# Kernel optimization log

Hardware: AMD Instinct MI355X
Metric: run time of the kernel (lower is better)

The kernel has to match this reference:

```python
import jax, jax.numpy as jnp
import numpy as np
import math

EPS = 1e-8
MIN_RADIUS = 0.1
SINH_MAX = math.asinh(2.0 ** 15)
CURV = 1.0                     # exp(clamp(log(1.0), log(0.1), log(10)))
IMAGE_ALPHA = 0.25             # exp(clamp(log(1/4), max=0))
TEXT_ALPHA = 1.0 / 0.6         # exp(log(1/0.6)), frozen
LOGIT_SCALE = 1.0 / 0.07       # exp(clamp(log(1/0.07), max=4.6052))
ENTAIL_WEIGHT = 0.2


def exp_map0(x, curv):
    # MERU exponential map at the Lorentz-model origin (space components only).
    rc = jnp.sqrt(curv) * jnp.linalg.norm(x, axis=-1, keepdims=True)
    sinh_in = jnp.clip(rc, EPS, SINH_MAX)
    return jnp.sinh(sinh_in) * x / jnp.maximum(rc, EPS)


def pairwise_dist(x, y, curv):
    # x: (B,H,W,D) image feats on hyperboloid; y: (C,D) text protos. -> (B,H,W,C)
    x_time = jnp.sqrt(1.0 / curv + jnp.sum(x * x, axis=-1))   # (B,H,W)
    y_time = jnp.sqrt(1.0 / curv + jnp.sum(y * y, axis=-1))   # (C,)
    inner = jnp.einsum('bhwd,cd->bhwc', x, y) - x_time[..., None] * y_time
    c_xyl = -curv * inner
    return jnp.arccosh(jnp.maximum(c_xyl, 1.0 + EPS)) / jnp.sqrt(curv)


def oxy_angle(x, y, curv):
    # Exterior angle at x between origin->x and x->y geodesics. x,y: (...,D) -> (...,)
    x_time = jnp.sqrt(1.0 / curv + jnp.sum(x * x, axis=-1))
    y_time = jnp.sqrt(1.0 / curv + jnp.sum(y * y, axis=-1))
    c_xyl = curv * (jnp.sum(x * y, axis=-1) - x_time * y_time)
    acos_num = y_time + c_xyl * x_time
    acos_den = jnp.linalg.norm(x, axis=-1) * jnp.sqrt(jnp.maximum(c_xyl * c_xyl - 1.0, 0.0))
    acos_in = acos_num / (acos_den + EPS)
    return jnp.arccos(jnp.clip(acos_in, -1.0 + EPS, 1.0 - EPS))


def half_aperture(x, curv):
    asin_in = 2.0 * MIN_RADIUS / (jnp.linalg.norm(x, axis=-1) * jnp.sqrt(curv) + EPS)
    return jnp.arcsin(jnp.clip(asin_in, -1.0 + EPS, 1.0 - EPS))


def _forward(feats, text_protos, labels, mask):
    curv = jnp.float32(CURV)
    img = exp_map0(feats * IMAGE_ALPHA, curv)          # (B,H,W,D)
    txt = exp_map0(text_protos * TEXT_ALPHA, curv)     # (C,D)

    dist = pairwise_dist(img, txt, curv)               # (B,H,W,C)
    proto = txt[labels]                                # (B,H,W,D) gather by GT class
    angle = oxy_angle(proto, img, curv)                # (B,H,W)
    aperture = half_aperture(proto, curv)              # (B,H,W)

    logits = LOGIT_SCALE * (-dist)                     # scale * image_logits
    logp = jax.nn.log_softmax(logits, axis=-1)
    nll = -jnp.take_along_axis(logp, labels[..., None], axis=-1)[..., 0]

    valid = (~mask).astype(jnp.float32)                # mask==1 means ignore
    n_valid = jnp.maximum(jnp.sum(valid), 1.0)
    sup_loss = jnp.sum(nll * valid) / n_valid

    ent = jnp.maximum(angle - aperture, 0.0)
    entail_loss = jnp.sum(ent * valid) / n_valid

    return sup_loss + ENTAIL_WEIGHT * entail_loss


def setup_inputs() -> dict:
    key = jax.random.key(0)
    k1, k2, k3, k4 = jax.random.split(key, 4)
    B, H, W, D, C = 2, 512, 512, 64, 151
    feats = jax.random.normal(k1, (B, H, W, D), dtype=jnp.float32)
    text_protos = jax.random.normal(k2, (C, D), dtype=jnp.float32)
    labels = jax.random.randint(k3, (B, H, W), 0, C, dtype=jnp.int32)
    mask = jax.random.randint(k4, (B, H, W), 0, 2, dtype=jnp.int32).astype(bool)
    return {"feats": feats, "text_protos": text_protos, "labels": labels, "mask": mask}


def reference(feats, text_protos, labels, mask):
    return _forward(feats, text_protos, labels, mask)
```

## Files before the change

kernel.cpp:

```cpp
#include <hip/hip_runtime.h>
#include <math.h>

#define EPSF 1e-8f
#define SINH_MAXF 11.090354888959125f
#define IMAGE_ALPHA 0.25f
#define TEXT_ALPHA (1.0f/0.6f)
#define LOGIT_SCALE (1.0f/0.07f)
#define LN2F 0.6931471805599453f
#define SLN (LOGIT_SCALE*LN2F)
#define ENTAIL_WEIGHT 0.2f
#define NCLS 151
#define NPAD 160
#define DIM 64
#define NBLK 2048

#define LMIN_OFF 8
#define YT_OFF 16
#define XN_OFF (YT_OFF + NPAD)
#define AP_OFF (XN_OFF + NPAD)
#define BT_OFF 512
#define BLK_OFF (BT_OFF + NPAD*DIM/2)

#if __has_builtin(__builtin_amdgcn_exp2f)
#define EXP2F(x) __builtin_amdgcn_exp2f(x)
#else
#define EXP2F(x) __expf((x) * LN2F)
#endif

typedef __attribute__((ext_vector_type(8))) short bf16x8;
typedef __attribute__((ext_vector_type(4))) float f32x4;

__device__ inline unsigned short f2bf(float f) {
    unsigned int u = __float_as_uint(f);
    return (unsigned short)((u + 0x7FFFu + ((u >> 16) & 1u)) >> 16);
}
__device__ inline unsigned int pack_bf_trunc(float hi, float lo) {
    return __builtin_amdgcn_perm(__float_as_uint(hi), __float_as_uint(lo), 0x07060302u);
}
__device__ inline float sel4(const float* a, int i) {
    return i == 0 ? a[0] : i == 1 ? a[1] : i == 2 ? a[2] : a[3];
}
__device__ inline int isel4(const int* a, int i) {
    return i == 0 ? a[0] : i == 1 ? a[1] : i == 2 ? a[2] : a[3];
}

__global__ __launch_bounds__(256) void proto_kernel(const float* __restrict__ protos,
                                                    float* __restrict__ ws) {
    int tid = threadIdx.x;
    int grp = tid >> 4, li = tid & 15;
    unsigned int* btu = (unsigned int*)(ws + BT_OFF);
    __shared__ float sYT[NPAD];
    #pragma unroll 2
    for (int t = 0; t < 10; t++) {
        int c = t * 16 + grp;
        float4 p4 = make_float4(0.f, 0.f, 0.f, 0.f);
        if (c < NCLS) p4 = ((const float4*)protos)[c * 16 + li];
        float vx = p4.x * TEXT_ALPHA, vy = p4.y * TEXT_ALPHA,
              vz = p4.z * TEXT_ALPHA, vw = p4.w * TEXT_ALPHA;
        float n2 = vx*vx + vy*vy + vz*vz + vw*vw;
        #pragma unroll
        for (int m = 8; m >= 1; m >>= 1) n2 += __shfl_xor(n2, m, 64);
        float rc = __builtin_amdgcn_sqrtf(n2);
        float rr = fminf(fmaxf(rc, EPSF), SINH_MAXF);
        float e = __expf(rr);
        float sh = 0.5f * (e - __builtin_amdgcn_rcpf(e));
        float sc = sh * __builtin_amdgcn_rcpf(fmaxf(rc, EPSF));
        unsigned int u0, u1;
        float yt, xn, ap;
        if (c < NCLS) {
            u0 = (unsigned int)f2bf(sc * vx) | ((unsigned int)f2bf(sc * vy) << 16);
            u1 = (unsigned int)f2bf(sc * vz) | ((unsigned int)f2bf(sc * vw) << 16);
            xn = sc * rc;
            yt = __builtin_amdgcn_sqrtf(fmaf(xn, xn, 1.f));
            float ai = fminf(fmaxf(0.2f / (xn + EPSF), -1.f + EPSF), 1.f - EPSF);
            ap = asinf(ai);
        } else {
            u0 = 0u; u1 = 0u; yt = 2e18f; xn = 1.f; ap = 0.f;
        }
        int unit = t * 128 + (li >> 3) * 64 + ((li >> 1) & 3) * 16 + grp;
        btu[unit * 4 + (li & 1) * 2]     = u0;
        btu[unit * 4 + (li & 1) * 2 + 1] = u1;
        if (li == 0) {
            ws[YT_OFF + c] = yt; ws[XN_OFF + c] = xn; ws[AP_OFF + c] = ap;
            sYT[c] = yt;
        }
    }
    __syncthreads();
    if (tid < 64) {
        float m = 1e30f;
        for (int c = tid; c < NCLS; c += 64) m = fminf(m, sYT[c]);
        #pragma unroll
        for (int k = 32; k >= 1; k >>= 1) m = fminf(m, __shfl_xor(m, k, 64));
        if (tid == 0) ws[LMIN_OFF] = __log2f(2.f * m);
    }
}

struct PixA { bf16x8 q0, q1; float xt, Q; };

__device__ inline PixA stage_pixel(const float4* fp, float lmin2) {
    float4 f0 = fp[0], f1 = fp[1], f2 = fp[8], f3 = fp[9];
    float n2r = f0.x*f0.x + f0.y*f0.y + f0.z*f0.z + f0.w*f0.w
              + f1.x*f1.x + f1.y*f1.y + f1.z*f1.z + f1.w*f1.w
              + f2.x*f2.x + f2.y*f2.y + f2.z*f2.z + f2.w*f2.w
              + f3.x*f3.x + f3.y*f3.y + f3.z*f3.z + f3.w*f3.w;
    n2r += __shfl_xor(n2r, 16, 64);
    n2r += __shfl_xor(n2r, 32, 64);
    float rc = IMAGE_ALPHA * __builtin_amdgcn_sqrtf(n2r);
    float rr = fminf(fmaxf(rc, EPSF), SINH_MAXF);
    float e = __expf(rr);
    float sh = 0.5f * (e - __builtin_amdgcn_rcpf(e));
    float sc = sh * __builtin_amdgcn_rcpf(fmaxf(rc, EPSF));
    float xn = sc * rc;
    float k = sc * IMAGE_ALPHA;
    PixA r;
    r.xt = __builtin_amdgcn_sqrtf(fmaf(xn, xn, 1.f));
    r.Q = LOGIT_SCALE * (lmin2 - __log2f(r.xt + xn) - 1.0f);
    unsigned int* q0u = (unsigned int*)&r.q0;
    unsigned int* q1u = (unsigned int*)&r.q1;
    q0u[0] = pack_bf_trunc(k*f0.y, k*f0.x);
    q0u[1] = pack_bf_trunc(k*f0.w, k*f0.z);
    q0u[2] = pack_bf_trunc(k*f1.y, k*f1.x);
    q0u[3] = pack_bf_trunc(k*f1.w, k*f1.z);
    q1u[0] = pack_bf_trunc(k*f2.y, k*f2.x);
    q1u[1] = pack_bf_trunc(k*f2.w, k*f2.z);
    q1u[2] = pack_bf_trunc(k*f3.y, k*f3.x);
    q1u[3] = pack_bf_trunc(k*f3.w, k*f3.z);
    return r;
}

__global__ __launch_bounds__(256) void main_kernel(
    const float* __restrict__ feats, const int* __restrict__ labels,
    const unsigned char* __restrict__ mask, const float* __restrict__ wsro,
    float4* __restrict__ blkout, int nchunk)
{
    __shared__ uint4 sBT[1280];
    __shared__ float sYT[NPAD];
    int tid = threadIdx.x;
    const uint4* btg = (const uint4*)(wsro + BT_OFF);
    #pragma unroll
    for (int k = 0; k < 5; k++) sBT[tid + k * 256] = btg[tid + k * 256];
    if (tid < NPAD) sYT[tid] = wsro[YT_OFF + tid];
    __syncthreads();

    int wid = tid >> 6, lane = tid & 63;
    int cn = lane & 15, g = lane >> 4;
    float lmin2 = wsro[LMIN_OFF];

    float v_nll = 0.f, v_ent = 0.f, valid = 0.f;

    for (int chunk = blockIdx.x; chunk < nchunk; chunk += NBLK) {
        int wavebase = (chunk * 4 + wid) * 32;
        int pix0 = wavebase + cn, pix1 = pix0 + 16;

        PixA A0 = stage_pixel((const float4*)(feats + (size_t)pix0 * DIM + g * 8), lmin2);
        PixA A1 = stage_pixel((const float4*)(feats + (size_t)pix1 * DIM + g * 8), lmin2);
        int lab0 = labels[pix0], lab1 = labels[pix1];

        float xtr0[4], Q0[4], xtr1[4], Q1[4];
        int lr0[4], lr1[4];
        #pragma unroll
        for (int r = 0; r < 4; r++) {
            int src = g * 4 + r;
            xtr0[r] = __shfl(A0.xt, src, 64); Q0[r] = __shfl(A0.Q, src, 64);
            lr0[r]  = __shfl(lab0, src, 64);
            xtr1[r] = __shfl(A1.xt, src, 64); Q1[r] = __shfl(A1.Q, src, 64);
            lr1[r]  = __shfl(lab1, src, 64);
        }

        float ss0[4] = {0,0,0,0}, ss1[4] = {0,0,0,0};
        float sv0[4] = {0,0,0,0}, sv1[4] = {0,0,0,0};

        #pragma unroll 2
        for (int t = 0; t < 10; t++) {
            uint4 u0 = sBT[t * 128 + lane];
            uint4 u1 = sBT[t * 128 + 64 + lane];
            bf16x8 bq0 = __builtin_bit_cast(bf16x8, u0);
            bf16x8 bq1 = __builtin_bit_cast(bf16x8, u1);
            float yt = sYT[t * 16 + cn];
            int cls = t * 16 + cn;
            f32x4 d0 = {0,0,0,0}, d1 = {0,0,0,0};
            d0 = __builtin_amdgcn_mfma_f32_16x16x32_bf16(A0.q0, bq0, d0, 0, 0, 0);
            d0 = __builtin_amdgcn_mfma_f32_16x16x32_bf16(A0.q1, bq1, d0, 0, 0, 0);
            d1 = __builtin_amdgcn_mfma_f32_16x16x32_bf16(A1.q0, bq0, d1, 0, 0, 0);
            d1 = __builtin_amdgcn_mfma_f32_16x16x32_bf16(A1.q1, bq1, d1, 0, 0, 0);
            #pragma unroll
            for (int r = 0; r < 4; r++) {
                float c0 = fmaf(xtr0[r], yt, -d0[r]);
                if (lr0[r] == cls) sv0[r] = c0;
                ss0[r] += EXP2F(fmaf(-LOGIT_SCALE, __log2f(c0), Q0[r]));
                float c1 = fmaf(xtr1[r], yt, -d1[r]);
                if (lr1[r] == cls) sv1[r] = c1;
                ss1[r] += EXP2F(fmaf(-LOGIT_SCALE, __log2f(c1), Q1[r]));
            }
        }

        int gbase = lane & 48;
        float cx0[4], cx1[4];
        #pragma unroll
        for (int r = 0; r < 4; r++) {
            cx0[r] = __shfl(sv0[r], gbase + (lr0[r] & 15), 64);
            cx1[r] = __shfl(sv1[r], gbase + (lr1[r] & 15), 64);
        }
        #pragma unroll
        for (int k = 1; k < 16; k <<= 1) {
            #pragma unroll
            for (int r = 0; r < 4; r++) {
                ss0[r] += __shfl_xor(ss0[r], k, 64);
                ss1[r] += __shfl_xor(ss1[r], k, 64);
            }
        }

        if (cn < 4) {
            #pragma unroll
            for (int tile = 0; tile < 2; tile++) {
                float T   = tile ? sel4(ss1, cn) : sel4(ss0, cn);
                float cxl = tile ? sel4(cx1, cn) : sel4(cx0, cn);
                float xts = tile ? sel4(xtr1, cn) : sel4(xtr0, cn);
                float Q   = tile ? sel4(Q1, cn) : sel4(Q0, cn);
                int lb    = tile ? isel4(lr1, cn) : isel4(lr0, cn);
                int pr = wavebase + g * 4 + cn + tile * 16;
                float nll = LN2F * (__log2f(T) - Q + LOGIT_SCALE * __log2f(cxl));
                float pt = wsro[YT_OFF + lb], pn = wsro[XN_OFF + lb], ap = wsro[AP_OFF + lb];
                float num = fmaf(-cxl, pt, xts);
                float den = pn * __builtin_amdgcn_sqrtf(fmaxf(fmaf(cxl, cxl, -1.f), 0.f));
                float ain = num * __builtin_amdgcn_rcpf(den + EPSF);
                ain = fminf(fmaxf(ain, -1.f + EPSF), 1.f - EPSF);
                float ax = fabsf(ain);
                float p = fmaf(fmaf(fmaf(-0.0187293f, ax, 0.0742610f), ax, -0.2121144f),
                               ax, 1.5707288f);
                float rr = __builtin_amdgcn_sqrtf(1.f - ax) * p;
                float ac = ain < 0.f ? 3.14159265358979f - rr : rr;
                float ent = fmaxf(ac - ap, 0.f);
                float vl = mask[pr] ? 0.f : 1.f;
                v_nll += nll * vl; v_ent += ent * vl; valid += vl;
            }
        }
    }

    #pragma unroll
    for (int o = 32; o >= 1; o >>= 1) {
        v_nll += __shfl_down(v_nll, o, 64);
        v_ent += __shfl_down(v_ent, o, 64);
        valid += __shfl_down(valid, o, 64);
    }
    __shared__ float red[3][4];
    if (lane == 0) { red[0][wid] = v_nll; red[1][wid] = v_ent; red[2][wid] = valid; }
    __syncthreads();
    if (tid == 0) {
        float a = 0.f, b = 0.f, c = 0.f;
        #pragma unroll
        for (int w = 0; w < 4; w++) { a += red[0][w]; b += red[1][w]; c += red[2][w]; }
        blkout[blockIdx.x] = make_float4(a, b, c, 0.f);
    }
}

__global__ __launch_bounds__(1024) void reduce_kernel(const float4* __restrict__ blk,
                                                      float* __restrict__ out) {
    float a = 0.f, b = 0.f, c = 0.f;
    for (int i = threadIdx.x; i < NBLK; i += 1024) {
        float4 v = blk[i];
        a += v.x; b += v.y; c += v.z;
    }
    #pragma unroll
    for (int o = 32; o >= 1; o >>= 1) {
        a += __shfl_down(a, o, 64);
        b += __shfl_down(b, o, 64);
        c += __shfl_down(c, o, 64);
    }
    __shared__ float red[3][16];
    int wid = threadIdx.x >> 6, lane = threadIdx.x & 63;
    if (lane == 0) { red[0][wid] = a; red[1][wid] = b; red[2][wid] = c; }
    __syncthreads();
    if (threadIdx.x == 0) {
        float A = 0.f, B = 0.f, C = 0.f;
        #pragma unroll
        for (int w = 0; w < 16; w++) { A += red[0][w]; B += red[1][w]; C += red[2][w]; }
        float n = fmaxf(C, 1.f);
        out[0] = A / n + ENTAIL_WEIGHT * (B / n);
    }
}

extern "C" void kernel_launch(void* const* d_in, const int* in_sizes, int n_in,
                              void* d_out, int out_size, void* d_ws, size_t ws_size,
                              hipStream_t stream) {
    const float* feats  = (const float*)d_in[0];
    const float* protos = (const float*)d_in[1];
    const int* labels   = (const int*)d_in[2];
    const unsigned char* mask = (const unsigned char*)d_in[3];
    float* ws = (float*)d_ws;

    proto_kernel<<<1, 256, 0, stream>>>(protos, ws);

    int npix = in_sizes[2];
    int nchunk = npix / 128;
    main_kernel<<<NBLK, 256, 0, stream>>>(feats, labels, mask, ws,
                                          (float4*)(ws + BLK_OFF), nchunk);
    reduce_kernel<<<1, 1024, 0, stream>>>((const float4*)(ws + BLK_OFF), (float*)d_out);
}
```

Baseline: 212.3 us.

## Prefetch both chunks' inputs before LDS staging, two chunks per block

```diff
diff --git a/kernel.cpp b/kernel.cpp
--- a/kernel.cpp
+++ b/kernel.cpp
@@ -97,8 +97,8 @@
 
 struct PixA { bf16x8 q0, q1; float xt, Q; };
 
-__device__ inline PixA stage_pixel(const float4* fp, float lmin2) {
-    float4 f0 = fp[0], f1 = fp[1], f2 = fp[8], f3 = fp[9];
+__device__ __forceinline__ PixA stage_pixel_r(float4 f0, float4 f1, float4 f2, float4 f3,
+                                              float lmin2) {
     float n2r = f0.x*f0.x + f0.y*f0.y + f0.z*f0.z + f0.w*f0.w
               + f1.x*f1.x + f1.y*f1.y + f1.z*f1.z + f1.w*f1.w
               + f2.x*f2.x + f2.y*f2.y + f2.z*f2.z + f2.w*f2.w
@@ -128,7 +128,98 @@
     return r;
 }
 
-__global__ __launch_bounds__(256) void main_kernel(
+__device__ __forceinline__ void process_chunk(
+    float4 a00, float4 a01, float4 a02, float4 a03,
+    float4 a10, float4 a11, float4 a12, float4 a13,
+    int lab0, int lab1, unsigned char mk0, unsigned char mk1,
+    int lane, int cn, int g,
+    const uint4* sBT, const float* sYT, const float* __restrict__ wsro, float lmin2,
+    float& v_nll, float& v_ent, float& valid)
+{
+    PixA A0 = stage_pixel_r(a00, a01, a02, a03, lmin2);
+    PixA A1 = stage_pixel_r(a10, a11, a12, a13, lmin2);
+
+    float xtr0[4], Q0[4], xtr1[4], Q1[4];
+    int lr0[4], lr1[4];
+    #pragma unroll
+    for (int r = 0; r < 4; r++) {
+        int src = g * 4 + r;
+        xtr0[r] = __shfl(A0.xt, src, 64); Q0[r] = __shfl(A0.Q, src, 64);
+        lr0[r]  = __shfl(lab0, src, 64);
+        xtr1[r] = __shfl(A1.xt, src, 64); Q1[r] = __shfl(A1.Q, src, 64);
+        lr1[r]  = __shfl(lab1, src, 64);
+    }
+
+    float ss0[4] = {0,0,0,0}, ss1[4] = {0,0,0,0};
+    float sv0[4] = {0,0,0,0}, sv1[4] = {0,0,0,0};
+
+    #pragma unroll 2
+    for (int t = 0; t < 10; t++) {
+        uint4 u0 = sBT[t * 128 + lane];
+        uint4 u1 = sBT[t * 128 + 64 + lane];
+        bf16x8 bq0 = __builtin_bit_cast(bf16x8, u0);
+        bf16x8 bq1 = __builtin_bit_cast(bf16x8, u1);
+        float yt = sYT[t * 16 + cn];
+        int cls = t * 16 + cn;
+        f32x4 d0 = {0,0,0,0}, d1 = {0,0,0,0};
+        d0 = __builtin_amdgcn_mfma_f32_16x16x32_bf16(A0.q0, bq0, d0, 0, 0, 0);
+        d0 = __builtin_amdgcn_mfma_f32_16x16x32_bf16(A0.q1, bq1, d0, 0, 0, 0);
+        d1 = __builtin_amdgcn_mfma_f32_16x16x32_bf16(A1.q0, bq0, d1, 0, 0, 0);
+        d1 = __builtin_amdgcn_mfma_f32_16x16x32_bf16(A1.q1, bq1, d1, 0, 0, 0);
+        #pragma unroll
+        for (int r = 0; r < 4; r++) {
+            float c0 = fmaf(xtr0[r], yt, -d0[r]);
+            if (lr0[r] == cls) sv0[r] = c0;
+            ss0[r] += EXP2F(fmaf(-LOGIT_SCALE, __log2f(c0), Q0[r]));
+            float c1 = fmaf(xtr1[r], yt, -d1[r]);
+            if (lr1[r] == cls) sv1[r] = c1;
+            ss1[r] += EXP2F(fmaf(-LOGIT_SCALE, __log2f(c1), Q1[r]));
+        }
+    }
+
+    int gbase = lane & 48;
+    float cx0[4], cx1[4];
+    #pragma unroll
+    for (int r = 0; r < 4; r++) {
+        cx0[r] = __shfl(sv0[r], gbase + (lr0[r] & 15), 64);
+        cx1[r] = __shfl(sv1[r], gbase + (lr1[r] & 15), 64);
+    }
+    #pragma unroll
+    for (int k = 1; k < 16; k <<= 1) {
+        #pragma unroll
+        for (int r = 0; r < 4; r++) {
+            ss0[r] += __shfl_xor(ss0[r], k, 64);
+            ss1[r] += __shfl_xor(ss1[r], k, 64);
+        }
+    }
+
+    if (cn < 4) {
+        #pragma unroll
+        for (int tile = 0; tile < 2; tile++) {
+            float T   = tile ? sel4(ss1, cn) : sel4(ss0, cn);
+            float cxl = tile ? sel4(cx1, cn) : sel4(cx0, cn);
+            float xts = tile ? sel4(xtr1, cn) : sel4(xtr0, cn);
+            float Q   = tile ? sel4(Q1, cn) : sel4(Q0, cn);
+            int lb    = tile ? isel4(lr1, cn) : isel4(lr0, cn);
+            float nll = LN2F * (__log2f(T) - Q + LOGIT_SCALE * __log2f(cxl));
+            float pt = wsro[YT_OFF + lb], pn = wsro[XN_OFF + lb], ap = wsro[AP_OFF + lb];
+            float num = fmaf(-cxl, pt, xts);
+            float den = pn * __builtin_amdgcn_sqrtf(fmaxf(fmaf(cxl, cxl, -1.f), 0.f));
+            float ain = num * __builtin_amdgcn_rcpf(den + EPSF);
+            ain = fminf(fmaxf(ain, -1.f + EPSF), 1.f - EPSF);
+            float ax = fabsf(ain);
+            float p = fmaf(fmaf(fmaf(-0.0187293f, ax, 0.0742610f), ax, -0.2121144f),
+                           ax, 1.5707288f);
+            float rr = __builtin_amdgcn_sqrtf(1.f - ax) * p;
+            float ac = ain < 0.f ? 3.14159265358979f - rr : rr;
+            float ent = fmaxf(ac - ap, 0.f);
+            float vl = (tile ? mk1 : mk0) ? 0.f : 1.f;
+            v_nll += nll * vl; v_ent += ent * vl; valid += vl;
+        }
+    }
+}
+
+__global__ __launch_bounds__(256, 4) void main_kernel(
     const float* __restrict__ feats, const int* __restrict__ labels,
     const unsigned char* __restrict__ mask, const float* __restrict__ wsro,
     float4* __restrict__ blkout, int nchunk)
@@ -136,106 +227,53 @@
     __shared__ uint4 sBT[1280];
     __shared__ float sYT[NPAD];
     int tid = threadIdx.x;
+    int wid = tid >> 6, lane = tid & 63;
+    int cn = lane & 15, g = lane >> 4;
+
+    int chunkA = blockIdx.x * 2;
+    int chunkB = chunkA + 1;
+    bool haveB = chunkB < nchunk;
+
+    int wbA = (chunkA * 4 + wid) * 32;
+    int pA0 = wbA + cn, pA1 = pA0 + 16;
+    const float4* fA0 = (const float4*)(feats + (size_t)pA0 * DIM + g * 8);
+    const float4* fA1 = (const float4*)(feats + (size_t)pA1 * DIM + g * 8);
+    float4 a00 = fA0[0], a01 = fA0[1], a02 = fA0[8], a03 = fA0[9];
+    float4 a10 = fA1[0], a11 = fA1[1], a12 = fA1[8], a13 = fA1[9];
+    int labA0 = labels[pA0], labA1 = labels[pA1];
+    unsigned char mkA0 = mask[wbA + g * 4 + cn], mkA1 = mask[wbA + g * 4 + cn + 16];
+
+    int wbB = (chunkB * 4 + wid) * 32;
+    float4 b00, b01, b02, b03, b10, b11, b12, b13;
+    int labB0 = 0, labB1 = 0;
+    unsigned char mkB0 = 1, mkB1 = 1;
+    b00 = b01 = b02 = b03 = b10 = b11 = b12 = b13 = make_float4(0.f, 0.f, 0.f, 0.f);
+    if (haveB) {
+        int pB0 = wbB + cn, pB1 = pB0 + 16;
+        const float4* fB0 = (const float4*)(feats + (size_t)pB0 * DIM + g * 8);
+        const float4* fB1 = (const float4*)(feats + (size_t)pB1 * DIM + g * 8);
+        b00 = fB0[0]; b01 = fB0[1]; b02 = fB0[8]; b03 = fB0[9];
+        b10 = fB1[0]; b11 = fB1[1]; b12 = fB1[8]; b13 = fB1[9];
+        labB0 = labels[pB0]; labB1 = labels[pB1];
+        mkB0 = mask[wbB + g * 4 + cn]; mkB1 = mask[wbB + g * 4 + cn + 16];
+    }
+    __builtin_amdgcn_sched_barrier(0);
+
     const uint4* btg = (const uint4*)(wsro + BT_OFF);
     #pragma unroll
     for (int k = 0; k < 5; k++) sBT[tid + k * 256] = btg[tid + k * 256];
     if (tid < NPAD) sYT[tid] = wsro[YT_OFF + tid];
     __syncthreads();
-
-    int wid = tid >> 6, lane = tid & 63;
-    int cn = lane & 15, g = lane >> 4;
     float lmin2 = wsro[LMIN_OFF];
 
     float v_nll = 0.f, v_ent = 0.f, valid = 0.f;
-
-    for (int chunk = blockIdx.x; chunk < nchunk; chunk += NBLK) {
-        int wavebase = (chunk * 4 + wid) * 32;
-        int pix0 = wavebase + cn, pix1 = pix0 + 16;
-
-        PixA A0 = stage_pixel((const float4*)(feats + (size_t)pix0 * DIM + g * 8), lmin2);
-        PixA A1 = stage_pixel((const float4*)(feats + (size_t)pix1 * DIM + g * 8), lmin2);
-        int lab0 = labels[pix0], lab1 = labels[pix1];
-
-        float xtr0[4], Q0[4], xtr1[4], Q1[4];
-        int lr0[4], lr1[4];
-        #pragma unroll
-        for (int r = 0; r < 4; r++) {
-            int src = g * 4 + r;
-            xtr0[r] = __shfl(A0.xt, src, 64); Q0[r] = __shfl(A0.Q, src, 64);
-            lr0[r]  = __shfl(lab0, src, 64);
-            xtr1[r] = __shfl(A1.xt, src, 64); Q1[r] = __shfl(A1.Q, src, 64);
-            lr1[r]  = __shfl(lab1, src, 64);
-        }
-
-        float ss0[4] = {0,0,0,0}, ss1[4] = {0,0,0,0};
-        float sv0[4] = {0,0,0,0}, sv1[4] = {0,0,0,0};
-
-        #pragma unroll 2
-        for (int t = 0; t < 10; t++) {
-            uint4 u0 = sBT[t * 128 + lane];
-            uint4 u1 = sBT[t * 128 + 64 + lane];
-            bf16x8 bq0 = __builtin_bit_cast(bf16x8, u0);
-            bf16x8 bq1 = __builtin_bit_cast(bf16x8, u1);
-            float yt = sYT[t * 16 + cn];
-            int cls = t * 16 + cn;
-            f32x4 d0 = {0,0,0,0}, d1 = {0,0,0,0};
-            d0 = __builtin_amdgcn_mfma_f32_16x16x32_bf16(A0.q0, bq0, d0, 0, 0, 0);
-            d0 = __builtin_amdgcn_mfma_f32_16x16x32_bf16(A0.q1, bq1, d0, 0, 0, 0);
-            d1 = __builtin_amdgcn_mfma_f32_16x16x32_bf16(A1.q0, bq0, d1, 0, 0, 0);
-            d1 = __builtin_amdgcn_mfma_f32_16x16x32_bf16(A1.q1, bq1, d1, 0, 0, 0);
-            #pragma unroll
-            for (int r = 0; r < 4; r++) {
-                float c0 = fmaf(xtr0[r], yt, -d0[r]);
-                if (lr0[r] == cls) sv0[r] = c0;
-                ss0[r] += EXP2F(fmaf(-LOGIT_SCALE, __log2f(c0), Q0[r]));
-                float c1 = fmaf(xtr1[r], yt, -d1[r]);
-                if (lr1[r] == cls) sv1[r] = c1;
-                ss1[r] += EXP2F(fmaf(-LOGIT_SCALE, __log2f(c1), Q1[r]));
-            }
-        }
-
-        int gbase = lane & 48;
-        float cx0[4], cx1[4];
-        #pragma unroll
-        for (int r = 0; r < 4; r++) {
-            cx0[r] = __shfl(sv0[r], gbase + (lr0[r] & 15), 64);
-            cx1[r] = __shfl(sv1[r], gbase + (lr1[r] & 15), 64);
-        }
-        #pragma unroll
-        for (int k = 1; k < 16; k <<= 1) {
-            #pragma unroll
-            for (int r = 0; r < 4; r++) {
-                ss0[r] += __shfl_xor(ss0[r], k, 64);
-                ss1[r] += __shfl_xor(ss1[r], k, 64);
-            }
-        }
-
-        if (cn < 4) {
-            #pragma unroll
-            for (int tile = 0; tile < 2; tile++) {
-                float T   = tile ? sel4(ss1, cn) : sel4(ss0, cn);
-                float cxl = tile ? sel4(cx1, cn) : sel4(cx0, cn);
-                float xts = tile ? sel4(xtr1, cn) : sel4(xtr0, cn);
-                float Q   = tile ? sel4(Q1, cn) : sel4(Q0, cn);
-                int lb    = tile ? isel4(lr1, cn) : isel4(lr0, cn);
-                int pr = wavebase + g * 4 + cn + tile * 16;
-                float nll = LN2F * (__log2f(T) - Q + LOGIT_SCALE * __log2f(cxl));
-                float pt = wsro[YT_OFF + lb], pn = wsro[XN_OFF + lb], ap = wsro[AP_OFF + lb];
-                float num = fmaf(-cxl, pt, xts);
-                float den = pn * __builtin_amdgcn_sqrtf(fmaxf(fmaf(cxl, cxl, -1.f), 0.f));
-                float ain = num * __builtin_amdgcn_rcpf(den + EPSF);
-                ain = fminf(fmaxf(ain, -1.f + EPSF), 1.f - EPSF);
-                float ax = fabsf(ain);
-                float p = fmaf(fmaf(fmaf(-0.0187293f, ax, 0.0742610f), ax, -0.2121144f),
-                               ax, 1.5707288f);
-                float rr = __builtin_amdgcn_sqrtf(1.f - ax) * p;
-                float ac = ain < 0.f ? 3.14159265358979f - rr : rr;
-                float ent = fmaxf(ac - ap, 0.f);
-                float vl = mask[pr] ? 0.f : 1.f;
-                v_nll += nll * vl; v_ent += ent * vl; valid += vl;
-            }
-        }
-    }
+    process_chunk(a00, a01, a02, a03, a10, a11, a12, a13,
+                  labA0, labA1, mkA0, mkA1, lane, cn, g,
+                  sBT, sYT, wsro, lmin2, v_nll, v_ent, valid);
+    if (haveB)
+        process_chunk(b00, b01, b02, b03, b10, b11, b12, b13,
+                      labB0, labB1, mkB0, mkB1, lane, cn, g,
+                      sBT, sYT, wsro, lmin2, v_nll, v_ent, valid);
 
     #pragma unroll
     for (int o = 32; o >= 1; o >>= 1) {
```

Result: slower. 225.4 us (+6.2%).
